# Kernel tuning notes

Hardware: AMD Instinct MI355X
Metric: run time of the kernel (lower is better)

## Reference

```python
import jax, jax.numpy as jnp
import numpy as np
from jax import lax

D_MODEL = 1024
D_FF = 4096
NUM_EXPERTS = 24
TOP_K = 2
B, S = 2, 2048


def setup_inputs() -> dict:
    key = jax.random.key(0)
    ks = jax.random.split(key, 5)
    x = jax.random.normal(ks[0], (B, S, D_MODEL), dtype=jnp.float32)
    gate_w = jax.random.normal(ks[1], (D_MODEL, NUM_EXPERTS), dtype=jnp.float32) * 0.02
    gate_b = jnp.zeros((NUM_EXPERTS,), dtype=jnp.float32)
    w1 = jax.random.normal(ks[2], (NUM_EXPERTS, D_MODEL, D_FF), dtype=jnp.float32) * 0.02
    b1 = jnp.zeros((NUM_EXPERTS, D_FF), dtype=jnp.float32)
    w2 = jax.random.normal(ks[3], (NUM_EXPERTS, D_FF, D_MODEL), dtype=jnp.float32) * 0.02
    b2 = jnp.zeros((NUM_EXPERTS, D_MODEL), dtype=jnp.float32)
    return {"x": x, "gate_w": gate_w, "gate_b": gate_b,
            "w1": w1, "b1": b1, "w2": w2, "b2": b2}


def reference(x, gate_w, gate_b, w1, b1, w2, b2):
    b, s, d = x.shape
    t = b * s
    xf = x.reshape(t, d)  # [T, d]
    scores = xf @ gate_w + gate_b  # [T, E]
    top_val, top_idx = lax.top_k(scores, TOP_K)  # [T, k]
    prob = jax.nn.softmax(top_val, axis=-1)  # softmax over the top-k logits
    # scatter top-k probabilities into dense per-expert combine weights [T, E]
    combine = jnp.zeros((t, NUM_EXPERTS), dtype=x.dtype)
    combine = combine.at[jnp.arange(t)[:, None], top_idx].add(prob)

    def body(acc, expert):
        w1e, b1e, w2e, b2e, ce = expert  # ce: [T]
        h = jax.nn.gelu(xf @ w1e + b1e, approximate=False)  # exact GELU as torch default
        y = h @ w2e + b2e  # [T, d]
        return acc + ce[:, None] * y, None

    out, _ = lax.scan(body, jnp.zeros_like(xf), (w1, b1, w2, b2, combine.T))
    return out.reshape(b, s, d)
```

## Files before the change

kernel.cpp:

```cpp
#include <hip/hip_runtime.h>
#include <math.h>

#define DM 1024
#define DF 4096
#define NE 24
#define T_TOK 4096
#define T2 (T_TOK*2)

#define BM 128
#define BN 64
#define BK 64
#define MTILES 8
#define NK1 (DM / BK)
#define NK2 (DF / BK)

typedef __attribute__((ext_vector_type(4))) float f32x4;
typedef __attribute__((ext_vector_type(8))) short s16x8;

static __device__ __forceinline__ unsigned short f2bf(float f) {
    unsigned int u = __float_as_uint(f);
    unsigned int r = u + 0x7fffu + ((u >> 16) & 1u);
    return (unsigned short)(r >> 16);
}

#define GLL(gsrc, ldst)                                                          \
    __builtin_amdgcn_global_load_lds(                                            \
        (const __attribute__((address_space(1))) void*)(gsrc),                   \
        (__attribute__((address_space(3))) void*)(ldst), 16, 0, 0)


__global__ void k_transpose_gw(const float* __restrict__ gw, float* __restrict__ gwT) {
    int e = blockIdx.x;
    for (int d = threadIdx.x; d < DM; d += blockDim.x)
        gwT[e * DM + d] = gw[d * NE + e];
}

__global__ void k_gate(const float* __restrict__ x, const float* __restrict__ gwT,
                       const float* __restrict__ gb,
                       int* __restrict__ idx, float* __restrict__ prob) {
    int wave = threadIdx.x >> 6;
    int lane = threadIdx.x & 63;
    int t = blockIdx.x * 4 + wave;
    if (t >= T_TOK) return;
    const float* xr = x + (size_t)t * DM;
    float acc[NE];
#pragma unroll
    for (int e = 0; e < NE; e++) acc[e] = 0.f;
    for (int i = 0; i < DM / 64; i++) {
        int d = lane + i * 64;
        float xv = xr[d];
#pragma unroll
        for (int e = 0; e < NE; e++) acc[e] = fmaf(xv, gwT[e * DM + d], acc[e]);
    }
#pragma unroll
    for (int e = 0; e < NE; e++) {
        float v = acc[e];
        for (int off = 32; off >= 1; off >>= 1) v += __shfl_xor(v, off);
        acc[e] = v;
    }
    if (lane == 0) {
        float v1 = -1e30f, v2 = -1e30f;
        int i1 = -1, i2 = -1;
        for (int e = 0; e < NE; e++) {
            float s = acc[e] + gb[e];
            if (s > v1) { v2 = v1; i2 = i1; v1 = s; i1 = e; }
            else if (s > v2) { v2 = s; i2 = e; }
        }
        float e2 = expf(v2 - v1);
        float inv = 1.f / (1.f + e2);
        idx[t * 2] = i1; idx[t * 2 + 1] = i2;
        prob[t * 2] = inv; prob[t * 2 + 1] = e2 * inv;
    }
}


__global__ __launch_bounds__(1024)
void k_route(const int* __restrict__ idx, int* __restrict__ counts,
             int* __restrict__ offsets, int* __restrict__ slot_tok,
             int* __restrict__ pair_slot) {
    __shared__ int cnt[NE], offs[NE], cur[NE];
    const int tid = threadIdx.x;
    if (tid < NE) cnt[tid] = 0;
    __syncthreads();
    for (int i = tid; i < T2; i += 1024) atomicAdd(&cnt[idx[i]], 1);
    __syncthreads();
    if (tid == 0) {
        int s = 0;
        for (int e = 0; e < NE; e++) {
            offs[e] = s; offsets[e] = s; counts[e] = cnt[e]; s += cnt[e];
        }
    }
    if (tid < NE) cur[tid] = 0;
    __syncthreads();
    for (int i = tid; i < T2; i += 1024) {
        int e = idx[i];
        int pos = offs[e] + atomicAdd(&cur[e], 1);
        slot_tok[pos] = i >> 1;
        pair_slot[i] = pos;
    }
}

__global__ void k_gather(const float* __restrict__ x, const int* __restrict__ slot_tok,
                         unsigned short* __restrict__ Xg) {
    int s = blockIdx.x;
    int tok = slot_tok[s];
    const float4* src = (const float4*)(x + (size_t)tok * DM);
    ushort4* dst = (ushort4*)(Xg + (size_t)s * DM);
    for (int i = threadIdx.x; i < DM / 4; i += blockDim.x) {
        float4 v = src[i];
        ushort4 o;
        o.x = f2bf(v.x); o.y = f2bf(v.y); o.z = f2bf(v.z); o.w = f2bf(v.w);
        dst[i] = o;
    }
}

__global__ void k_combine(const float* __restrict__ Y, const int* __restrict__ pair_slot,
                          const float* __restrict__ prob, const int* __restrict__ idx,
                          const float* __restrict__ b2, float* __restrict__ out) {
    int t = blockIdx.x;
    int s1 = pair_slot[t * 2], s2 = pair_slot[t * 2 + 1];
    int e1 = idx[t * 2], e2 = idx[t * 2 + 1];
    float p1 = prob[t * 2], p2 = prob[t * 2 + 1];
    const float4* y1 = (const float4*)(Y + (size_t)s1 * DM);
    const float4* y2 = (const float4*)(Y + (size_t)s2 * DM);
    const float4* ba = (const float4*)(b2 + (size_t)e1 * DM);
    const float4* bb = (const float4*)(b2 + (size_t)e2 * DM);
    float4* o = (float4*)(out + (size_t)t * DM);
    int i = threadIdx.x;
    float4 a = y1[i], b = y2[i], c = ba[i], d = bb[i];
    float4 r;
    r.x = p1 * (a.x + c.x) + p2 * (b.x + d.x);
    r.y = p1 * (a.y + c.y) + p2 * (b.y + d.y);
    r.z = p1 * (a.z + c.z) + p2 * (b.z + d.z);
    r.w = p1 * (a.w + c.w) + p2 * (b.w + d.w);
    o[i] = r;
}


__global__ __launch_bounds__(256)
void k_mm1(const unsigned short* __restrict__ Xg, const float* __restrict__ w1,
           const float* __restrict__ b1, const int* __restrict__ counts,
           const int* __restrict__ offsets, unsigned short* __restrict__ H) {
    const int TOT = NE * MTILES * (DF / BN);
    int work = (blockIdx.x & 7) * (TOT >> 3) + (blockIdx.x >> 3);
    const int mt = work % MTILES;
    const int en = work / MTILES;
    const int e  = en >> 6;
    const int n0 = (en & 63) * BN;
    const int ne = counts[e];
    const int m0 = mt * BM;
    if (m0 >= ne) return;
    const int rows = min(BM, ne - m0);
    const int slotbase = offsets[e] + m0;

    __shared__ unsigned short As[BM * BK];
    __shared__ float          Bf[BN * BK];
    __shared__ unsigned short Bs[BN * BK];

    const int tid  = threadIdx.x;
    const int lane = tid & 63;
    const int w    = tid >> 6;
    const int wm   = w >> 1, wn = w & 1;

    const float* w1e = w1 + (size_t)e * DM * DF;
    const int arow = lane >> 3;
    const int gchunk = ((lane & 7) ^ arow) * 8;

    const int swz0 = ((lane >> 4) ^ (lane & 7)) << 4;
    const int swz1 = ((4 | (lane >> 4)) ^ (lane & 7)) << 4;
    const char* Arow = (const char*)As + (wm * 64 + (lane & 15)) * 128;
    const char* Brow = (const char*)Bs + (wn * 32 + (lane & 15)) * 128;

    const int cn = lane;
    const int ck = w * 16;
    const int cc0 = ((ck >> 3) ^ (cn & 7)) << 4;
    const int cc1 = (((ck >> 3) + 1) ^ (cn & 7)) << 4;
    char* BsRowC = (char*)Bs + cn * 128;

    f32x4 acc[4][2];
#pragma unroll
    for (int a = 0; a < 4; a++)
#pragma unroll
        for (int b = 0; b < 2; b++) acc[a][b] = (f32x4)0.f;

#pragma unroll 1
    for (int kt = 0; kt < NK1; ++kt) {
        const int k0 = kt * BK;
#pragma unroll
        for (int q = 0; q < 4; q++) {
            int row = (w * 4 + q) * 8 + arow;
            GLL(Xg + (size_t)(slotbase + row) * DM + k0 + gchunk,
                &As[(w * 4 + q) * 512]);
        }
#pragma unroll
        for (int q = 0; q < 4; q++) {
            GLL(w1e + (size_t)(k0 + w * 16 + q * 4 + (lane >> 4)) * DF + n0 + (lane & 15) * 4,
                &Bf[(w * 16 + q * 4) * 64]);
        }
        __syncthreads();
        s16x8 af[2][4];
#pragma unroll
        for (int f = 0; f < 4; f++) {
            af[0][f] = *(const s16x8*)(Arow + f * 2048 + swz0);
            af[1][f] = *(const s16x8*)(Arow + f * 2048 + swz1);
        }
        {
            s16x8 v0, v1;
#pragma unroll
            for (int j = 0; j < 8; j++)
                v0[j] = (short)f2bf(Bf[(ck + j) * 64 + cn]);
#pragma unroll
            for (int j = 0; j < 8; j++)
                v1[j] = (short)f2bf(Bf[(ck + 8 + j) * 64 + cn]);
            *(s16x8*)(BsRowC + cc0) = v0;
            *(s16x8*)(BsRowC + cc1) = v1;
        }
        __syncthreads();
        s16x8 bfr[2][2];
#pragma unroll
        for (int f = 0; f < 2; f++) {
            bfr[0][f] = *(const s16x8*)(Brow + f * 2048 + swz0);
            bfr[1][f] = *(const s16x8*)(Brow + f * 2048 + swz1);
        }
#pragma unroll
        for (int ks = 0; ks < 2; ks++)
#pragma unroll
            for (int fm = 0; fm < 4; fm++)
#pragma unroll
                for (int fn = 0; fn < 2; fn++)
                    acc[fm][fn] = __builtin_amdgcn_mfma_f32_16x16x32_bf16(
                        af[ks][fm], bfr[ks][fn], acc[fm][fn], 0, 0, 0);
        __syncthreads();
    }

    const float* b1e = b1 + (size_t)e * DF;
#pragma unroll
    for (int fm = 0; fm < 4; fm++) {
        const int mrow = wm * 64 + fm * 16 + ((lane >> 4) << 2);
#pragma unroll
        for (int fn = 0; fn < 2; fn++) {
            const int ncol = n0 + wn * 32 + fn * 16 + (lane & 15);
            const float bb = b1e[ncol];
#pragma unroll
            for (int r = 0; r < 4; r++) {
                const int m = mrow + r;
                if (m < rows) {
                    float h = acc[fm][fn][r] + bb;
                    h = 0.5f * h * (1.f + erff(h * 0.70710678118654752f));
                    H[(size_t)(slotbase + m) * DF + ncol] = f2bf(h);
                }
            }
        }
    }
}

__global__ __launch_bounds__(256)
void k_mm2(const unsigned short* __restrict__ Hb, const float* __restrict__ w2,
           const int* __restrict__ counts, const int* __restrict__ offsets,
           float* __restrict__ Y) {
    const int TOT = NE * MTILES * (DM / BN);
    int work = (blockIdx.x & 7) * (TOT >> 3) + (blockIdx.x >> 3);
    const int mt = work % MTILES;
    const int en = work / MTILES;
    const int e  = en >> 4;
    const int n0 = (en & 15) * BN;
    const int ne = counts[e];
    const int m0 = mt * BM;
    if (m0 >= ne) return;
    const int rows = min(BM, ne - m0);
    const int slotbase = offsets[e] + m0;

    __shared__ unsigned short As[BM * BK];
    __shared__ float          Bf[BN * BK];
    __shared__ unsigned short Bs[BN * BK];

    const int tid  = threadIdx.x;
    const int lane = tid & 63;
    const int w    = tid >> 6;
    const int wm   = w >> 1, wn = w & 1;

    const float* w2e = w2 + (size_t)e * DF * DM;
    const int arow = lane >> 3;
    const int gchunk = ((lane & 7) ^ arow) * 8;

    const int swz0 = ((lane >> 4) ^ (lane & 7)) << 4;
    const int swz1 = ((4 | (lane >> 4)) ^ (lane & 7)) << 4;
    const char* Arow = (const char*)As + (wm * 64 + (lane & 15)) * 128;
    const char* Brow = (const char*)Bs + (wn * 32 + (lane & 15)) * 128;

    const int cn = lane;
    const int ck = w * 16;
    const int cc0 = ((ck >> 3) ^ (cn & 7)) << 4;
    const int cc1 = (((ck >> 3) + 1) ^ (cn & 7)) << 4;
    char* BsRowC = (char*)Bs + cn * 128;

    f32x4 acc[4][2];
#pragma unroll
    for (int a = 0; a < 4; a++)
#pragma unroll
        for (int b = 0; b < 2; b++) acc[a][b] = (f32x4)0.f;

#pragma unroll 1
    for (int kt = 0; kt < NK2; ++kt) {
        const int k0 = kt * BK;
#pragma unroll
        for (int q = 0; q < 4; q++) {
            int row = (w * 4 + q) * 8 + arow;
            GLL(Hb + (size_t)(slotbase + row) * DF + k0 + gchunk,
                &As[(w * 4 + q) * 512]);
        }
#pragma unroll
        for (int q = 0; q < 4; q++) {
            GLL(w2e + (size_t)(k0 + w * 16 + q * 4 + (lane >> 4)) * DM + n0 + (lane & 15) * 4,
                &Bf[(w * 16 + q * 4) * 64]);
        }
        __syncthreads();
        s16x8 af[2][4];
#pragma unroll
        for (int f = 0; f < 4; f++) {
            af[0][f] = *(const s16x8*)(Arow + f * 2048 + swz0);
            af[1][f] = *(const s16x8*)(Arow + f * 2048 + swz1);
        }
        {
            s16x8 v0, v1;
#pragma unroll
            for (int j = 0; j < 8; j++)
                v0[j] = (short)f2bf(Bf[(ck + j) * 64 + cn]);
#pragma unroll
            for (int j = 0; j < 8; j++)
                v1[j] = (short)f2bf(Bf[(ck + 8 + j) * 64 + cn]);
            *(s16x8*)(BsRowC + cc0) = v0;
            *(s16x8*)(BsRowC + cc1) = v1;
        }
        __syncthreads();
        s16x8 bfr[2][2];
#pragma unroll
        for (int f = 0; f < 2; f++) {
            bfr[0][f] = *(const s16x8*)(Brow + f * 2048 + swz0);
            bfr[1][f] = *(const s16x8*)(Brow + f * 2048 + swz1);
        }
#pragma unroll
        for (int ks = 0; ks < 2; ks++)
#pragma unroll
            for (int fm = 0; fm < 4; fm++)
#pragma unroll
                for (int fn = 0; fn < 2; fn++)
                    acc[fm][fn] = __builtin_amdgcn_mfma_f32_16x16x32_bf16(
                        af[ks][fm], bfr[ks][fn], acc[fm][fn], 0, 0, 0);
        __syncthreads();
    }

#pragma unroll
    for (int fm = 0; fm < 4; fm++) {
        const int mrow = wm * 64 + fm * 16 + ((lane >> 4) << 2);
#pragma unroll
        for (int fn = 0; fn < 2; fn++) {
            const int ncol = n0 + wn * 32 + fn * 16 + (lane & 15);
#pragma unroll
            for (int r = 0; r < 4; r++) {
                const int m = mrow + r;
                if (m < rows)
                    Y[(size_t)(slotbase + m) * DM + ncol] = acc[fm][fn][r];
            }
        }
    }
}


extern "C" void kernel_launch(void* const* d_in, const int* in_sizes, int n_in,
                              void* d_out, int out_size, void* d_ws, size_t ws_size,
                              hipStream_t stream) {
    const float* x   = (const float*)d_in[0];
    const float* gw  = (const float*)d_in[1];
    const float* gb  = (const float*)d_in[2];
    const float* w1  = (const float*)d_in[3];
    const float* b1  = (const float*)d_in[4];
    const float* w2  = (const float*)d_in[5];
    const float* b2  = (const float*)d_in[6];
    float* out = (float*)d_out;

    size_t off = 0;
    auto alloc = [&](size_t bytes) {
        void* p = (char*)d_ws + off;
        off += (bytes + 255) & ~(size_t)255;
        return p;
    };
    float* gwT       = (float*)alloc(NE * DM * sizeof(float));
    int*   idx       = (int*)alloc(T2 * sizeof(int));
    float* prob      = (float*)alloc(T2 * sizeof(float));
    int*   counts    = (int*)alloc(32 * sizeof(int));
    int*   offsets   = (int*)alloc(32 * sizeof(int));
    int*   slot_tok  = (int*)alloc(T2 * sizeof(int));
    int*   pair_slot = (int*)alloc(T2 * sizeof(int));
    unsigned short* Xg = (unsigned short*)alloc((size_t)(T2 + BM) * DM * sizeof(unsigned short));
    unsigned short* Hb = (unsigned short*)alloc((size_t)(T2 + BM) * DF * sizeof(unsigned short));
    float* Yb        = (float*)alloc((size_t)(T2 + BM) * DM * sizeof(float));

    k_transpose_gw<<<NE, 256, 0, stream>>>(gw, gwT);
    k_gate<<<T_TOK / 4, 256, 0, stream>>>(x, gwT, gb, idx, prob);
    k_route<<<1, 1024, 0, stream>>>(idx, counts, offsets, slot_tok, pair_slot);
    k_gather<<<T2, 256, 0, stream>>>(x, slot_tok, Xg);

    k_mm1<<<NE * MTILES * (DF / BN), 256, 0, stream>>>(Xg, w1, b1, counts, offsets, Hb);
    k_mm2<<<NE * MTILES * (DM / BN), 256, 0, stream>>>(Hb, w2, counts, offsets, Yb);
    k_combine<<<T_TOK, 256, 0, stream>>>(Yb, pair_slot, prob, idx, b2, out);
}
```

Measured before the change: 574.7 us.

## Double-buffer global-to-LDS loads in expert GEMMs and use packed bf16 conversion

Both expert GEMM kernels now keep two LDS buffers for the A tile and the fp32 B tile. The next k-tile's global_load_lds is issued before the current tile is computed, with explicit vmcnt waits and raw barriers, so global memory latency overlaps with MFMA work. The per-element fp32-to-bf16 rounding of the B tile is replaced with v_cvt_pk_bf16_f32, which converts two floats per instruction. In exchange, LDS use roughly doubles, which can lower occupancy, and the hand-written waitcnt counts must stay correct for the loads actually in flight.

Result: slower. 675.3 us (+17.5%).

```diff
diff --git a/kernel.cpp b/kernel.cpp
--- a/kernel.cpp
+++ b/kernel.cpp
@@ -21,6 +21,12 @@
     unsigned int u = __float_as_uint(f);
     unsigned int r = u + 0x7fffu + ((u >> 16) & 1u);
     return (unsigned short)(r >> 16);
+}
+
+static __device__ __forceinline__ unsigned int cvtpk(float lo, float hi) {
+    unsigned int r;
+    asm("v_cvt_pk_bf16_f32 %0, %1, %2" : "=v"(r) : "v"(lo), "v"(hi));
+    return r;
 }
 
 #define GLL(gsrc, ldst)                                                          \
@@ -153,8 +159,8 @@
     const int rows = min(BM, ne - m0);
     const int slotbase = offsets[e] + m0;
 
-    __shared__ unsigned short As[BM * BK];
-    __shared__ float          Bf[BN * BK];
+    __shared__ unsigned short As[2][BM * BK];
+    __shared__ float          Bf[2][BN * BK];
     __shared__ unsigned short Bs[BN * BK];
 
     const int tid  = threadIdx.x;
@@ -168,7 +174,8 @@
 
     const int swz0 = ((lane >> 4) ^ (lane & 7)) << 4;
     const int swz1 = ((4 | (lane >> 4)) ^ (lane & 7)) << 4;
-    const char* Arow = (const char*)As + (wm * 64 + (lane & 15)) * 128;
+    const char* Arow0 = (const char*)As[0] + (wm * 64 + (lane & 15)) * 128;
+    const char* Arow1 = (const char*)As[1] + (wm * 64 + (lane & 15)) * 128;
     const char* Brow = (const char*)Bs + (wn * 32 + (lane & 15)) * 128;
 
     const int cn = lane;
@@ -183,21 +190,33 @@
 #pragma unroll
         for (int b = 0; b < 2; b++) acc[a][b] = (f32x4)0.f;
 
-#pragma unroll 1
-    for (int kt = 0; kt < NK1; ++kt) {
-        const int k0 = kt * BK;
+    auto stage_pair = [&](int buf, int k0) {
 #pragma unroll
         for (int q = 0; q < 4; q++) {
             int row = (w * 4 + q) * 8 + arow;
             GLL(Xg + (size_t)(slotbase + row) * DM + k0 + gchunk,
-                &As[(w * 4 + q) * 512]);
+                &As[buf][(w * 4 + q) * 512]);
         }
 #pragma unroll
         for (int q = 0; q < 4; q++) {
             GLL(w1e + (size_t)(k0 + w * 16 + q * 4 + (lane >> 4)) * DF + n0 + (lane & 15) * 4,
-                &Bf[(w * 16 + q * 4) * 64]);
-        }
-        __syncthreads();
+                &Bf[buf][(w * 16 + q * 4) * 64]);
+        }
+    };
+
+    stage_pair(0, 0);
+#pragma unroll 1
+    for (int kt = 0; kt < NK1; ++kt) {
+        const int cur = kt & 1;
+        if (kt + 1 < NK1) {
+            stage_pair(cur ^ 1, (kt + 1) * BK);
+            asm volatile("s_waitcnt vmcnt(8)" ::: "memory");
+        } else {
+            asm volatile("s_waitcnt vmcnt(0)" ::: "memory");
+        }
+        __builtin_amdgcn_s_barrier();
+        __builtin_amdgcn_sched_barrier(0);
+        const char* Arow = cur ? Arow1 : Arow0;
         s16x8 af[2][4];
 #pragma unroll
         for (int f = 0; f < 4; f++) {
@@ -205,17 +224,22 @@
             af[1][f] = *(const s16x8*)(Arow + f * 2048 + swz1);
         }
         {
-            s16x8 v0, v1;
-#pragma unroll
-            for (int j = 0; j < 8; j++)
-                v0[j] = (short)f2bf(Bf[(ck + j) * 64 + cn]);
-#pragma unroll
-            for (int j = 0; j < 8; j++)
-                v1[j] = (short)f2bf(Bf[(ck + 8 + j) * 64 + cn]);
-            *(s16x8*)(BsRowC + cc0) = v0;
-            *(s16x8*)(BsRowC + cc1) = v1;
-        }
-        __syncthreads();
+            const float* bf = Bf[cur];
+            uint4 v0, v1;
+            v0.x = cvtpk(bf[(ck + 0) * 64 + cn], bf[(ck + 1) * 64 + cn]);
+            v0.y = cvtpk(bf[(ck + 2) * 64 + cn], bf[(ck + 3) * 64 + cn]);
+            v0.z = cvtpk(bf[(ck + 4) * 64 + cn], bf[(ck + 5) * 64 + cn]);
+            v0.w = cvtpk(bf[(ck + 6) * 64 + cn], bf[(ck + 7) * 64 + cn]);
+            v1.x = cvtpk(bf[(ck + 8) * 64 + cn], bf[(ck + 9) * 64 + cn]);
+            v1.y = cvtpk(bf[(ck + 10) * 64 + cn], bf[(ck + 11) * 64 + cn]);
+            v1.z = cvtpk(bf[(ck + 12) * 64 + cn], bf[(ck + 13) * 64 + cn]);
+            v1.w = cvtpk(bf[(ck + 14) * 64 + cn], bf[(ck + 15) * 64 + cn]);
+            *(uint4*)(BsRowC + cc0) = v0;
+            *(uint4*)(BsRowC + cc1) = v1;
+        }
+        asm volatile("s_waitcnt lgkmcnt(0)" ::: "memory");
+        __builtin_amdgcn_s_barrier();
+        __builtin_amdgcn_sched_barrier(0);
         s16x8 bfr[2][2];
 #pragma unroll
         for (int f = 0; f < 2; f++) {
@@ -230,7 +254,9 @@
                 for (int fn = 0; fn < 2; fn++)
                     acc[fm][fn] = __builtin_amdgcn_mfma_f32_16x16x32_bf16(
                         af[ks][fm], bfr[ks][fn], acc[fm][fn], 0, 0, 0);
-        __syncthreads();
+        asm volatile("s_waitcnt lgkmcnt(0)" ::: "memory");
+        __builtin_amdgcn_s_barrier();
+        __builtin_amdgcn_sched_barrier(0);
     }
 
     const float* b1e = b1 + (size_t)e * DF;
@@ -270,8 +296,8 @@
     const int rows = min(BM, ne - m0);
     const int slotbase = offsets[e] + m0;
 
-    __shared__ unsigned short As[BM * BK];
-    __shared__ float          Bf[BN * BK];
+    __shared__ unsigned short As[2][BM * BK];
+    __shared__ float          Bf[2][BN * BK];
     __shared__ unsigned short Bs[BN * BK];
 
     const int tid  = threadIdx.x;
@@ -285,7 +311,8 @@
 
     const int swz0 = ((lane >> 4) ^ (lane & 7)) << 4;
     const int swz1 = ((4 | (lane >> 4)) ^ (lane & 7)) << 4;
-    const char* Arow = (const char*)As + (wm * 64 + (lane & 15)) * 128;
+    const char* Arow0 = (const char*)As[0] + (wm * 64 + (lane & 15)) * 128;
+    const char* Arow1 = (const char*)As[1] + (wm * 64 + (lane & 15)) * 128;
     const char* Brow = (const char*)Bs + (wn * 32 + (lane & 15)) * 128;
 
     const int cn = lane;
@@ -300,21 +327,33 @@
 #pragma unroll
         for (int b = 0; b < 2; b++) acc[a][b] = (f32x4)0.f;
 
-#pragma unroll 1
-    for (int kt = 0; kt < NK2; ++kt) {
-        const int k0 = kt * BK;
+    auto stage_pair = [&](int buf, int k0) {
 #pragma unroll
         for (int q = 0; q < 4; q++) {
             int row = (w * 4 + q) * 8 + arow;
             GLL(Hb + (size_t)(slotbase + row) * DF + k0 + gchunk,
-                &As[(w * 4 + q) * 512]);
+                &As[buf][(w * 4 + q) * 512]);
         }
 #pragma unroll
         for (int q = 0; q < 4; q++) {
             GLL(w2e + (size_t)(k0 + w * 16 + q * 4 + (lane >> 4)) * DM + n0 + (lane & 15) * 4,
-                &Bf[(w * 16 + q * 4) * 64]);
-        }
-        __syncthreads();
+                &Bf[buf][(w * 16 + q * 4) * 64]);
+        }
+    };
+
+    stage_pair(0, 0);
+#pragma unroll 1
+    for (int kt = 0; kt < NK2; ++kt) {
+        const int cur = kt & 1;
+        if (kt + 1 < NK2) {
+            stage_pair(cur ^ 1, (kt + 1) * BK);
+            asm volatile("s_waitcnt vmcnt(8)" ::: "memory");
+        } else {
+            asm volatile("s_waitcnt vmcnt(0)" ::: "memory");
+        }
+        __builtin_amdgcn_s_barrier();
+        __builtin_amdgcn_sched_barrier(0);
+        const char* Arow = cur ? Arow1 : Arow0;
         s16x8 af[2][4];
 #pragma unroll
         for (int f = 0; f < 4; f++) {
@@ -322,17 +361,22 @@
             af[1][f] = *(const s16x8*)(Arow + f * 2048 + swz1);
         }
         {
-            s16x8 v0, v1;
-#pragma unroll
-            for (int j = 0; j < 8; j++)
-                v0[j] = (short)f2bf(Bf[(ck + j) * 64 + cn]);
-#pragma unroll
-            for (int j = 0; j < 8; j++)
-                v1[j] = (short)f2bf(Bf[(ck + 8 + j) * 64 + cn]);
-            *(s16x8*)(BsRowC + cc0) = v0;
-            *(s16x8*)(BsRowC + cc1) = v1;
-        }
-        __syncthreads();
+            const float* bf = Bf[cur];
+            uint4 v0, v1;
+            v0.x = cvtpk(bf[(ck + 0) * 64 + cn], bf[(ck + 1) * 64 + cn]);
+            v0.y = cvtpk(bf[(ck + 2) * 64 + cn], bf[(ck + 3) * 64 + cn]);
+            v0.z = cvtpk(bf[(ck + 4) * 64 + cn], bf[(ck + 5) * 64 + cn]);
+            v0.w = cvtpk(bf[(ck + 6) * 64 + cn], bf[(ck + 7) * 64 + cn]);
+            v1.x = cvtpk(bf[(ck + 8) * 64 + cn], bf[(ck + 9) * 64 + cn]);
+            v1.y = cvtpk(bf[(ck + 10) * 64 + cn], bf[(ck + 11) * 64 + cn]);
+            v1.z = cvtpk(bf[(ck + 12) * 64 + cn], bf[(ck + 13) * 64 + cn]);
+            v1.w = cvtpk(bf[(ck + 14) * 64 + cn], bf[(ck + 15) * 64 + cn]);
+            *(uint4*)(BsRowC + cc0) = v0;
+            *(uint4*)(BsRowC + cc1) = v1;
+        }
+        asm volatile("s_waitcnt lgkmcnt(0)" ::: "memory");
+        __builtin_amdgcn_s_barrier();
+        __builtin_amdgcn_sched_barrier(0);
         s16x8 bfr[2][2];
 #pragma unroll
         for (int f = 0; f < 2; f++) {
@@ -347,7 +391,9 @@
                 for (int fn = 0; fn < 2; fn++)
                     acc[fm][fn] = __builtin_amdgcn_mfma_f32_16x16x32_bf16(
                         af[ks][fm], bfr[ks][fn], acc[fm][fn], 0, 0, 0);
-        __syncthreads();
+        asm volatile("s_waitcnt lgkmcnt(0)" ::: "memory");
+        __builtin_amdgcn_s_barrier();
+        __builtin_amdgcn_sched_barrier(0);
     }
 
 #pragma unroll
```
